# Performance work log

Measured on AMD Instinct MI355X. Metric: run time of the kernel, lower is better.

The kernel has to match this reference:

```python
import jax, jax.numpy as jnp
import numpy as np

SHARED = 128  # matches TabularLoss(shared=128)


def _pairwise_dist(x, y):
    """Batched pairwise L2 distances. x: (B,N,D), y: (B,M,D) -> (B,N,M)."""
    sq = (jnp.sum(x * x, axis=-1)[:, :, None]
          + jnp.sum(y * y, axis=-1)[:, None, :]
          - 2.0 * jnp.einsum('bnd,bmd->bnm', x, y))
    sq = jnp.maximum(sq, 0.0)
    # safe sqrt (exact forward, no NaN grads at 0)
    return jnp.where(sq > 0, jnp.sqrt(jnp.where(sq > 0, sq, 1.0)), 0.0)


def _energy_distance(x, y):
    """geomloss SamplesLoss(loss='energy') with uniform weights.
    L = <a, D_xy b> - 0.5 <a, D_xx a> - 0.5 <b, D_yy b>, a=b=1/N.
    Returns per-batch losses, shape (B,)."""
    dxy = jnp.mean(_pairwise_dist(x, y), axis=(-2, -1))
    dxx = jnp.mean(_pairwise_dist(x, x), axis=(-2, -1))
    dyy = jnp.mean(_pairwise_dist(y, y), axis=(-2, -1))
    return dxy - 0.5 * dxx - 0.5 * dyy


def setup_inputs() -> dict:
    key = jax.random.key(0)
    k1, k2 = jax.random.split(key)
    total, genes = 8192, 5000
    return {
        'input': jax.random.normal(k1, (total, genes), dtype=jnp.float32),
        'target': jax.random.normal(k2, (total, genes), dtype=jnp.float32),
        'downsample': 64,
    }


def reference(input, target, downsample):
    x = input.reshape(-1, downsample, input.shape[-1])   # (B, N, G)
    y = target.reshape(-1, downsample, target.shape[-1])
    # gene-level MMD: each cell group is a point cloud of N cells in G dims
    gene_mmd = jnp.nanmean(_energy_distance(x, y))
    # cell-level MMD: transpose(2,0) -> (S, N, B): per shared gene, N points in B dims
    cx = jnp.transpose(x[:, :, -SHARED:], (2, 1, 0))
    cy = jnp.transpose(y[:, :, -SHARED:], (2, 1, 0))
    cell_mmd = jnp.nanmean(_energy_distance(cx, cy))
    loss = (jnp.where(jnp.isnan(gene_mmd), 0.0, gene_mmd)
            + jnp.where(jnp.isnan(cell_mmd), 0.0, cell_mmd))
    return loss
```

## Files before the change

### kernel.cpp

```cpp
#include <hip/hip_runtime.h>
#include <math.h>

#define TOTAL   8192
#define GENES   5000
#define NDS     64
#define NB      128
#define NSHARED 128
#define KC      64

#define GRAM_OFF 64

typedef __attribute__((ext_vector_type(8)))  short          short8;
typedef __attribute__((ext_vector_type(4)))  unsigned short ushort4v;
typedef __attribute__((ext_vector_type(16))) float          f32x16;

static __device__ inline unsigned short f2bf(float f) {
    unsigned int u = __builtin_bit_cast(unsigned int, f);
    unsigned int r = (u + 0x7fffu + ((u >> 16) & 1u)) >> 16;
    return (unsigned short)r;
}
static __device__ inline float bf2f(unsigned short h) {
    unsigned int u = ((unsigned int)h) << 16;
    return __builtin_bit_cast(float, u);
}

__global__ __launch_bounds__(64) void k_zero(float* ws) {
    ws[threadIdx.x] = 0.0f;
}

__global__ __launch_bounds__(256) void k_gene_gram_mfma(const float* __restrict__ X,
                                                        const float* __restrict__ Y,
                                                        float* __restrict__ grams,
                                                        int splitD, int Dper) {
    const int blk = blockIdx.x;
    const int b = blk / splitD, c = blk % splitD;
    const int d0 = c * Dper;
    const int d1 = min(GENES, d0 + Dper);

    const float* __restrict__ xb = X + (size_t)b * NDS * GENES;
    const float* __restrict__ yb = Y + (size_t)b * NDS * GENES;

    __shared__ __align__(16) unsigned short sXh[NDS * KC], sXl[NDS * KC];
    __shared__ __align__(16) unsigned short sYh[NDS * KC], sYl[NDS * KC];

    const int t    = threadIdx.x;
    const int lane = t & 63;
    const int w    = t >> 6;
    const int qr   = w >> 1, qc = w & 1;
    const int lm   = lane & 31;
    const int kh   = (lane >> 5) << 3;

    const int mr = (qr << 5) + lm;
    const int mc = (qc << 5) + lm;

    f32x16 axy = {0,0,0,0,0,0,0,0,0,0,0,0,0,0,0,0};
    f32x16 axx = {0,0,0,0,0,0,0,0,0,0,0,0,0,0,0,0};
    f32x16 ayy = {0,0,0,0,0,0,0,0,0,0,0,0,0,0,0,0};

    for (int dd0 = d0; dd0 < d1; dd0 += KC) {
        __syncthreads();
#pragma unroll
        for (int it = 0; it < 4; ++it) {
            const int c4 = t & 15;
            const int m  = (t >> 4) + (it << 4);
            const int d  = dd0 + (c4 << 2);
            float vx[4] = {0.f, 0.f, 0.f, 0.f};
            float vy[4] = {0.f, 0.f, 0.f, 0.f};
            if (d + 3 < d1) {
                const float4 fx = *(const float4*)(xb + (size_t)m * GENES + d);
                const float4 fy = *(const float4*)(yb + (size_t)m * GENES + d);
                vx[0]=fx.x; vx[1]=fx.y; vx[2]=fx.z; vx[3]=fx.w;
                vy[0]=fy.x; vy[1]=fy.y; vy[2]=fy.z; vy[3]=fy.w;
            } else if (d < d1) {
                for (int q = 0; q < d1 - d; ++q) {
                    vx[q] = xb[(size_t)m * GENES + d + q];
                    vy[q] = yb[(size_t)m * GENES + d + q];
                }
            }
            ushort4v xh, xl, yh, yl;
#pragma unroll
            for (int q = 0; q < 4; ++q) {
                const unsigned short h = f2bf(vx[q]);
                xh[q] = h; xl[q] = f2bf(vx[q] - bf2f(h));
                const unsigned short g = f2bf(vy[q]);
                yh[q] = g; yl[q] = f2bf(vy[q] - bf2f(g));
            }
            const int e = m * KC + (((c4 << 2)) ^ ((m & 7) << 3));
            *(ushort4v*)&sXh[e] = xh;
            *(ushort4v*)&sXl[e] = xl;
            *(ushort4v*)&sYh[e] = yh;
            *(ushort4v*)&sYl[e] = yl;
        }
        __syncthreads();
#pragma unroll
        for (int ks = 0; ks < 4; ++ks) {
            const int kb = (ks << 4) + kh;
            const int er = mr * KC + (kb ^ ((mr & 7) << 3));
            const int ec = mc * KC + (kb ^ ((mc & 7) << 3));
            const short8 xhr = *(const short8*)&sXh[er];
            const short8 xlr = *(const short8*)&sXl[er];
            const short8 yhr = *(const short8*)&sYh[er];
            const short8 ylr = *(const short8*)&sYl[er];
            const short8 xhc = *(const short8*)&sXh[ec];
            const short8 xlc = *(const short8*)&sXl[ec];
            const short8 yhc = *(const short8*)&sYh[ec];
            const short8 ylc = *(const short8*)&sYl[ec];
            axy = __builtin_amdgcn_mfma_f32_32x32x16_bf16(xhr, yhc, axy, 0, 0, 0);
            axx = __builtin_amdgcn_mfma_f32_32x32x16_bf16(xhr, xhc, axx, 0, 0, 0);
            ayy = __builtin_amdgcn_mfma_f32_32x32x16_bf16(yhr, yhc, ayy, 0, 0, 0);
            axy = __builtin_amdgcn_mfma_f32_32x32x16_bf16(xhr, ylc, axy, 0, 0, 0);
            axx = __builtin_amdgcn_mfma_f32_32x32x16_bf16(xhr, xlc, axx, 0, 0, 0);
            ayy = __builtin_amdgcn_mfma_f32_32x32x16_bf16(yhr, ylc, ayy, 0, 0, 0);
            axy = __builtin_amdgcn_mfma_f32_32x32x16_bf16(xlr, yhc, axy, 0, 0, 0);
            axx = __builtin_amdgcn_mfma_f32_32x32x16_bf16(xlr, xhc, axx, 0, 0, 0);
            ayy = __builtin_amdgcn_mfma_f32_32x32x16_bf16(ylr, yhc, ayy, 0, 0, 0);
        }
    }

    float* g = grams + (size_t)(b * splitD + c) * 3 * 4096;
    const int col = (qc << 5) + lm;
#pragma unroll
    for (int r = 0; r < 16; ++r) {
        const int row = (qr << 5) + (r & 3) + ((r >> 2) << 3) + ((lane >> 5) << 2);
        g[0 * 4096 + row * 64 + col] = axy[r];
        g[1 * 4096 + row * 64 + col] = axx[r];
        g[2 * 4096 + row * 64 + col] = ayy[r];
    }
}

__global__ __launch_bounds__(256) void k_gene_dist(const float* __restrict__ grams,
                                                   float* __restrict__ acc,
                                                   int splitD) {
    const int b = blockIdx.x, t = threadIdx.x;
    __shared__ __align__(16) float G[3 * 4096];
    __shared__ float red[4];

    for (int m = 0; m < 3; ++m) {
#pragma unroll
        for (int k = 0; k < 16; ++k) {
            const int e = t + 256 * k;
            float s = 0.f;
            for (int c = 0; c < splitD; ++c)
                s += grams[((size_t)(b * splitD + c) * 3 + m) * 4096 + e];
            G[m * 4096 + e] = s;
        }
    }
    __syncthreads();

    float local = 0.f;
#pragma unroll
    for (int k = 0; k < 16; ++k) {
        const int e = t + 256 * k;
        const int i = e >> 6, j = e & 63;
        const float gxy = G[e];
        const float gxx = G[4096 + e];
        const float gyy = G[8192 + e];
        const float nxi = G[4096 + i * 65], nxj = G[4096 + j * 65];
        const float nyi = G[8192 + i * 65], nyj = G[8192 + j * 65];
        const float dxy = sqrtf(fmaxf(nxi + nyj - 2.f * gxy, 0.f));
        const float dxx = sqrtf(fmaxf(nxi + nxj - 2.f * gxx, 0.f));
        const float dyy = sqrtf(fmaxf(nyi + nyj - 2.f * gyy, 0.f));
        local += dxy - 0.5f * (dxx + dyy);
    }
#pragma unroll
    for (int off = 32; off; off >>= 1) local += __shfl_down(local, off);
    if ((t & 63) == 0) red[t >> 6] = local;
    __syncthreads();
    if (t == 0) {
        const float bl = red[0] + red[1] + red[2] + red[3];
        atomicAdd(acc, bl * (1.0f / (4096.0f * (float)NB)));
    }
}

__global__ __launch_bounds__(256) void k_cell(const float* __restrict__ X,
                                              const float* __restrict__ Y,
                                              float* __restrict__ acc) {
    const int s   = blockIdx.x;
    const int col = GENES - NSHARED + s;
    const int t   = threadIdx.x;

    __shared__ __align__(16) float lds[16384];

#pragma unroll
    for (int k = 0; k < 32; ++k) {
        const int idx = t + 256 * k;
        lds[idx]        = X[(size_t)idx * GENES + col];
        lds[8192 + idx] = Y[(size_t)idx * GENES + col];
    }
    __syncthreads();

    const int ti = t & 15, tj = t >> 4;
    const int i0 = ti << 2, j0 = tj << 2;
    float axy[4][4] = {{0}}, axx[4][4] = {{0}}, ayy[4][4] = {{0}};

#pragma unroll 4
    for (int bb = 0; bb < NB; ++bb) {
        const float4 xi4 = *(const float4*)(lds + bb * 64 + i0);
        const float4 xj4 = *(const float4*)(lds + bb * 64 + j0);
        const float4 yi4 = *(const float4*)(lds + 8192 + bb * 64 + i0);
        const float4 yj4 = *(const float4*)(lds + 8192 + bb * 64 + j0);
        const float* xi = &xi4.x;
        const float* xj = &xj4.x;
        const float* yi = &yi4.x;
        const float* yj = &yj4.x;
#pragma unroll
        for (int ii = 0; ii < 4; ++ii) {
#pragma unroll
            for (int jj = 0; jj < 4; ++jj) {
                axy[ii][jj] = fmaf(xi[ii], yj[jj], axy[ii][jj]);
                axx[ii][jj] = fmaf(xi[ii], xj[jj], axx[ii][jj]);
                ayy[ii][jj] = fmaf(yi[ii], yj[jj], ayy[ii][jj]);
            }
        }
    }
    __syncthreads();
#pragma unroll
    for (int ii = 0; ii < 4; ++ii) {
        float4 v;
        v.x = axy[ii][0]; v.y = axy[ii][1]; v.z = axy[ii][2]; v.w = axy[ii][3];
        *(float4*)(lds + 0 * 4096 + (i0 + ii) * 64 + j0) = v;
        v.x = axx[ii][0]; v.y = axx[ii][1]; v.z = axx[ii][2]; v.w = axx[ii][3];
        *(float4*)(lds + 1 * 4096 + (i0 + ii) * 64 + j0) = v;
        v.x = ayy[ii][0]; v.y = ayy[ii][1]; v.z = ayy[ii][2]; v.w = ayy[ii][3];
        *(float4*)(lds + 2 * 4096 + (i0 + ii) * 64 + j0) = v;
    }
    __syncthreads();

    float local = 0.f;
#pragma unroll
    for (int k = 0; k < 16; ++k) {
        const int e = t + 256 * k;
        const int i = e >> 6, j = e & 63;
        const float gxy = lds[e];
        const float gxx = lds[4096 + e];
        const float gyy = lds[8192 + e];
        const float nxi = lds[4096 + i * 65], nxj = lds[4096 + j * 65];
        const float nyi = lds[8192 + i * 65], nyj = lds[8192 + j * 65];
        const float dxy = sqrtf(fmaxf(nxi + nyj - 2.f * gxy, 0.f));
        const float dxx = sqrtf(fmaxf(nxi + nxj - 2.f * gxx, 0.f));
        const float dyy = sqrtf(fmaxf(nyi + nyj - 2.f * gyy, 0.f));
        local += dxy - 0.5f * (dxx + dyy);
    }
#pragma unroll
    for (int off = 32; off; off >>= 1) local += __shfl_down(local, off);
    __syncthreads();
    if ((t & 63) == 0) lds[t >> 6] = local;
    __syncthreads();
    if (t == 0) {
        const float bl = lds[0] + lds[1] + lds[2] + lds[3];
        atomicAdd(acc, bl * (1.0f / (4096.0f * (float)NSHARED)));
    }
}

__global__ void k_final(const float* __restrict__ acc, float* __restrict__ out) {
    out[0] = acc[0] + acc[1];
}

extern "C" void kernel_launch(void* const* d_in, const int* in_sizes, int n_in,
                              void* d_out, int out_size, void* d_ws, size_t ws_size,
                              hipStream_t stream) {
    const float* X = (const float*)d_in[0];
    const float* Y = (const float*)d_in[1];
    float* out = (float*)d_out;
    float* ws  = (float*)d_ws;

    int splitD = 4;
    while (splitD > 1 &&
           ((size_t)GRAM_OFF + (size_t)splitD * NB * 3 * 4096) * sizeof(float) > ws_size)
        splitD >>= 1;
    const int chunks = (GENES + KC - 1) / KC;
    const int cper   = (chunks + splitD - 1) / splitD;
    const int Dper   = cper * KC;

    float* acc   = ws;
    float* grams = ws + GRAM_OFF;

    hipLaunchKernelGGL(k_zero,           dim3(1),           dim3(64),  0, stream, acc);
    hipLaunchKernelGGL(k_gene_gram_mfma, dim3(NB * splitD), dim3(256), 0, stream,
                       X, Y, grams, splitD, Dper);
    hipLaunchKernelGGL(k_gene_dist,      dim3(NB),          dim3(256), 0, stream,
                       grams, acc + 0, splitD);
    hipLaunchKernelGGL(k_cell,           dim3(NSHARED),     dim3(256), 0, stream,
                       X, Y, acc + 1);
    hipLaunchKernelGGL(k_final,          dim3(1),           dim3(1),   0, stream, acc, out);
}
```

Before: 192.0 us.

## Prefetch next gene chunk into registers and pre-transpose shared columns for cell kernel

The gene Gram kernel now loads the next KC-wide chunk of X/Y into registers while the current chunk is split into bf16 hi/lo parts and run through the MFMAs, so global load latency overlaps compute. A new transpose kernel copies the last 128 columns of X and Y into a contiguous column-major buffer, reusing the gram workspace, after the gene distance kernel has consumed it. k_cell then does coalesced float4 loads instead of strided per-element column gathers. This adds an extra launch, an extra round trip through global memory, and more register pressure in the Gram kernel.

Result: slower. 235.2 us (+22.5%).

```diff
diff --git a/kernel.cpp b/kernel.cpp
--- a/kernel.cpp
+++ b/kernel.cpp
@@ -53,45 +53,66 @@
     const int mr = (qr << 5) + lm;
     const int mc = (qc << 5) + lm;
 
+    const int c4  = t & 15;
+    const int mrw = t >> 4;
+
     f32x16 axy = {0,0,0,0,0,0,0,0,0,0,0,0,0,0,0,0};
     f32x16 axx = {0,0,0,0,0,0,0,0,0,0,0,0,0,0,0,0};
     f32x16 ayy = {0,0,0,0,0,0,0,0,0,0,0,0,0,0,0,0};
 
-    for (int dd0 = d0; dd0 < d1; dd0 += KC) {
-        __syncthreads();
+    float4 rx[4], ry[4];
+
+    auto load_chunk = [&](int dd0) {
 #pragma unroll
         for (int it = 0; it < 4; ++it) {
-            const int c4 = t & 15;
-            const int m  = (t >> 4) + (it << 4);
-            const int d  = dd0 + (c4 << 2);
-            float vx[4] = {0.f, 0.f, 0.f, 0.f};
-            float vy[4] = {0.f, 0.f, 0.f, 0.f};
+            const int m = mrw + (it << 4);
+            const int d = dd0 + (c4 << 2);
+            float4 vx = {0.f, 0.f, 0.f, 0.f};
+            float4 vy = {0.f, 0.f, 0.f, 0.f};
             if (d + 3 < d1) {
-                const float4 fx = *(const float4*)(xb + (size_t)m * GENES + d);
-                const float4 fy = *(const float4*)(yb + (size_t)m * GENES + d);
-                vx[0]=fx.x; vx[1]=fx.y; vx[2]=fx.z; vx[3]=fx.w;
-                vy[0]=fy.x; vy[1]=fy.y; vy[2]=fy.z; vy[3]=fy.w;
+                vx = *(const float4*)(xb + (size_t)m * GENES + d);
+                vy = *(const float4*)(yb + (size_t)m * GENES + d);
             } else if (d < d1) {
+                float* px = &vx.x; float* py = &vy.x;
                 for (int q = 0; q < d1 - d; ++q) {
-                    vx[q] = xb[(size_t)m * GENES + d + q];
-                    vy[q] = yb[(size_t)m * GENES + d + q];
+                    px[q] = xb[(size_t)m * GENES + d + q];
+                    py[q] = yb[(size_t)m * GENES + d + q];
                 }
             }
-            ushort4v xh, xl, yh, yl;
+            rx[it] = vx; ry[it] = vy;
+        }
+    };
+
+    load_chunk(d0);
+
+    for (int dd0 = d0; dd0 < d1; dd0 += KC) {
+        ushort4v xh[4], xl[4], yh[4], yl[4];
+#pragma unroll
+        for (int it = 0; it < 4; ++it) {
+            const float* px = &rx[it].x;
+            const float* py = &ry[it].x;
 #pragma unroll
             for (int q = 0; q < 4; ++q) {
-                const unsigned short h = f2bf(vx[q]);
-                xh[q] = h; xl[q] = f2bf(vx[q] - bf2f(h));
-                const unsigned short g = f2bf(vy[q]);
-                yh[q] = g; yl[q] = f2bf(vy[q] - bf2f(g));
+                const unsigned short h = f2bf(px[q]);
+                xh[it][q] = h; xl[it][q] = f2bf(px[q] - bf2f(h));
+                const unsigned short g = f2bf(py[q]);
+                yh[it][q] = g; yl[it][q] = f2bf(py[q] - bf2f(g));
             }
-            const int e = m * KC + (((c4 << 2)) ^ ((m & 7) << 3));
-            *(ushort4v*)&sXh[e] = xh;
-            *(ushort4v*)&sXl[e] = xl;
-            *(ushort4v*)&sYh[e] = yh;
-            *(ushort4v*)&sYl[e] = yl;
-        }
+        }
+        if (dd0 + KC < d1) load_chunk(dd0 + KC);
+
         __syncthreads();
+#pragma unroll
+        for (int it = 0; it < 4; ++it) {
+            const int m = mrw + (it << 4);
+            const int e = m * KC + ((c4 << 2) ^ ((m & 7) << 3));
+            *(ushort4v*)&sXh[e] = xh[it];
+            *(ushort4v*)&sXl[e] = xl[it];
+            *(ushort4v*)&sYh[e] = yh[it];
+            *(ushort4v*)&sYl[e] = yl[it];
+        }
+        __syncthreads();
+
 #pragma unroll
         for (int ks = 0; ks < 4; ++ks) {
             const int kb = (ks << 4) + kh;
@@ -172,20 +193,57 @@
     }
 }
 
-__global__ __launch_bounds__(256) void k_cell(const float* __restrict__ X,
-                                              const float* __restrict__ Y,
+__global__ __launch_bounds__(256) void k_transpose(const float* __restrict__ X,
+                                                   const float* __restrict__ Y,
+                                                   float* __restrict__ T) {
+    const int blk = blockIdx.x;
+    const float* __restrict__ src = (blk < NB) ? X : Y;
+    float* __restrict__ dst = T + (size_t)(blk < NB ? 0 : NSHARED * TOTAL);
+    const int rb = (blk & (NB - 1)) * 64;
+    __shared__ float s[NSHARED * 65];
+    const int t = threadIdx.x;
+
+#pragma unroll
+    for (int it = 0; it < 8; ++it) {
+        const int idx = t + 256 * it;
+        const int r = idx >> 5;
+        const int f = idx & 31;
+        const float4 v = *(const float4*)(src + (size_t)(rb + r) * GENES
+                                          + (GENES - NSHARED) + (f << 2));
+        s[((f << 2) + 0) * 65 + r] = v.x;
+        s[((f << 2) + 1) * 65 + r] = v.y;
+        s[((f << 2) + 2) * 65 + r] = v.z;
+        s[((f << 2) + 3) * 65 + r] = v.w;
+    }
+    __syncthreads();
+
+    const int g = t >> 1, h = t & 1;
+#pragma unroll
+    for (int v = 0; v < 8; ++v) {
+        const int r = (h << 5) + (v << 2);
+        float4 o;
+        o.x = s[g * 65 + r + 0];
+        o.y = s[g * 65 + r + 1];
+        o.z = s[g * 65 + r + 2];
+        o.w = s[g * 65 + r + 3];
+        *(float4*)(dst + (size_t)g * TOTAL + rb + r) = o;
+    }
+}
+
+__global__ __launch_bounds__(256) void k_cell(const float* __restrict__ T,
                                               float* __restrict__ acc) {
-    const int s   = blockIdx.x;
-    const int col = GENES - NSHARED + s;
-    const int t   = threadIdx.x;
+    const int s = blockIdx.x;
+    const float* __restrict__ tx = T + (size_t)s * TOTAL;
+    const float* __restrict__ ty = T + (size_t)(NSHARED + s) * TOTAL;
+    const int t = threadIdx.x;
 
     __shared__ __align__(16) float lds[16384];
 
 #pragma unroll
-    for (int k = 0; k < 32; ++k) {
-        const int idx = t + 256 * k;
-        lds[idx]        = X[(size_t)idx * GENES + col];
-        lds[8192 + idx] = Y[(size_t)idx * GENES + col];
+    for (int it = 0; it < 8; ++it) {
+        const int i4 = (t + 256 * it) << 2;
+        *(float4*)&lds[i4]        = *(const float4*)(tx + i4);
+        *(float4*)&lds[8192 + i4] = *(const float4*)(ty + i4);
     }
     __syncthreads();
 
@@ -280,7 +338,9 @@
                        X, Y, grams, splitD, Dper);
     hipLaunchKernelGGL(k_gene_dist,      dim3(NB),          dim3(256), 0, stream,
                        grams, acc + 0, splitD);
+    hipLaunchKernelGGL(k_transpose,      dim3(2 * NB),      dim3(256), 0, stream,
+                       X, Y, grams);
     hipLaunchKernelGGL(k_cell,           dim3(NSHARED),     dim3(256), 0, stream,
-                       X, Y, acc + 1);
+                       grams, acc + 1);
     hipLaunchKernelGGL(k_final,          dim3(1),           dim3(1),   0, stream, acc, out);
 }
```

## Double-buffer LDS tiles and prefetch next chunk into registers during MFMA

Applied to the files above, without the earlier changes.

Adds a second LDS buffer for the bf16 hi/lo split tiles and issues the global loads for the next K-chunk into registers before the current chunk's MFMA work. The loaded data is converted and written to the alternate buffer after the MFMAs, so one barrier per chunk remains instead of two. The aim is to hide global-memory latency behind matrix math. In exchange it doubles LDS usage to 64KB per block and raises register pressure, which may lower occupancy.

New measurement: 225.3 us. +17.3%, slower.

```diff
diff --git a/kernel.cpp b/kernel.cpp
--- a/kernel.cpp
+++ b/kernel.cpp
@@ -40,8 +40,8 @@
     const float* __restrict__ xb = X + (size_t)b * NDS * GENES;
     const float* __restrict__ yb = Y + (size_t)b * NDS * GENES;
 
-    __shared__ __align__(16) unsigned short sXh[NDS * KC], sXl[NDS * KC];
-    __shared__ __align__(16) unsigned short sYh[NDS * KC], sYl[NDS * KC];
+    __shared__ __align__(16) unsigned short sXh[2 * NDS * KC], sXl[2 * NDS * KC];
+    __shared__ __align__(16) unsigned short sYh[2 * NDS * KC], sYl[2 * NDS * KC];
 
     const int t    = threadIdx.x;
     const int lane = t & 63;
@@ -53,50 +53,92 @@
     const int mr = (qr << 5) + lm;
     const int mc = (qc << 5) + lm;
 
+    const int c4  = t & 15;
+    const int mrw = t >> 4;
+    const int dcol = c4 << 2;
+
     f32x16 axy = {0,0,0,0,0,0,0,0,0,0,0,0,0,0,0,0};
     f32x16 axx = {0,0,0,0,0,0,0,0,0,0,0,0,0,0,0,0};
     f32x16 ayy = {0,0,0,0,0,0,0,0,0,0,0,0,0,0,0,0};
 
-    for (int dd0 = d0; dd0 < d1; dd0 += KC) {
-        __syncthreads();
-#pragma unroll
-        for (int it = 0; it < 4; ++it) {
-            const int c4 = t & 15;
-            const int m  = (t >> 4) + (it << 4);
-            const int d  = dd0 + (c4 << 2);
-            float vx[4] = {0.f, 0.f, 0.f, 0.f};
-            float vy[4] = {0.f, 0.f, 0.f, 0.f};
-            if (d + 3 < d1) {
-                const float4 fx = *(const float4*)(xb + (size_t)m * GENES + d);
-                const float4 fy = *(const float4*)(yb + (size_t)m * GENES + d);
-                vx[0]=fx.x; vx[1]=fx.y; vx[2]=fx.z; vx[3]=fx.w;
-                vy[0]=fy.x; vy[1]=fy.y; vy[2]=fy.z; vy[3]=fy.w;
-            } else if (d < d1) {
-                for (int q = 0; q < d1 - d; ++q) {
-                    vx[q] = xb[(size_t)m * GENES + d + q];
-                    vy[q] = yb[(size_t)m * GENES + d + q];
+    float4 rx0, rx1, rx2, rx3, ry0, ry1, ry2, ry3;
+
+    auto issue_loads = [&](int dd0) {
+        const int d = dd0 + dcol;
+        if (d + 3 < d1) {
+            const float* px = xb + (size_t)mrw * GENES + d;
+            const float* py = yb + (size_t)mrw * GENES + d;
+            rx0 = *(const float4*)(px);
+            ry0 = *(const float4*)(py);
+            rx1 = *(const float4*)(px + 16 * GENES);
+            ry1 = *(const float4*)(py + 16 * GENES);
+            rx2 = *(const float4*)(px + 32 * GENES);
+            ry2 = *(const float4*)(py + 32 * GENES);
+            rx3 = *(const float4*)(px + 48 * GENES);
+            ry3 = *(const float4*)(py + 48 * GENES);
+        } else {
+            float4 z = {0.f, 0.f, 0.f, 0.f};
+            rx0 = rx1 = rx2 = rx3 = z;
+            ry0 = ry1 = ry2 = ry3 = z;
+            if (d < d1) {
+                const int nq = d1 - d;
+                float* dstx[4] = {&rx0.x, &rx1.x, &rx2.x, &rx3.x};
+                float* dsty[4] = {&ry0.x, &ry1.x, &ry2.x, &ry3.x};
+#pragma unroll
+                for (int it = 0; it < 4; ++it) {
+                    const size_t base = (size_t)(mrw + (it << 4)) * GENES + d;
+                    for (int q = 0; q < nq; ++q) {
+                        dstx[it][q] = xb[base + q];
+                        dsty[it][q] = yb[base + q];
+                    }
                 }
             }
+        }
+    };
+
+    auto convert_write = [&](int buf) {
+        const int bofs = buf * NDS * KC;
+        const float4 vx[4] = {rx0, rx1, rx2, rx3};
+        const float4 vy[4] = {ry0, ry1, ry2, ry3};
+#pragma unroll
+        for (int it = 0; it < 4; ++it) {
+            const int m = mrw + (it << 4);
+            const float* px = &vx[it].x;
+            const float* py = &vy[it].x;
             ushort4v xh, xl, yh, yl;
 #pragma unroll
             for (int q = 0; q < 4; ++q) {
-                const unsigned short h = f2bf(vx[q]);
-                xh[q] = h; xl[q] = f2bf(vx[q] - bf2f(h));
-                const unsigned short g = f2bf(vy[q]);
-                yh[q] = g; yl[q] = f2bf(vy[q] - bf2f(g));
+                const unsigned short h = f2bf(px[q]);
+                xh[q] = h; xl[q] = f2bf(px[q] - bf2f(h));
+                const unsigned short g = f2bf(py[q]);
+                yh[q] = g; yl[q] = f2bf(py[q] - bf2f(g));
             }
-            const int e = m * KC + (((c4 << 2)) ^ ((m & 7) << 3));
+            const int e = bofs + m * KC + (dcol ^ ((m & 7) << 3));
             *(ushort4v*)&sXh[e] = xh;
             *(ushort4v*)&sXl[e] = xl;
             *(ushort4v*)&sYh[e] = yh;
             *(ushort4v*)&sYl[e] = yl;
         }
+    };
+
+    const int nchunks = (d1 - d0 + KC - 1) / KC;
+
+    issue_loads(d0);
+    convert_write(0);
+
+    for (int ci = 0; ci < nchunks; ++ci) {
+        const int cur = ci & 1;
+        const bool more = (ci + 1 < nchunks);
+        if (more) issue_loads(d0 + (ci + 1) * KC);
+
         __syncthreads();
+
+        const int bofs = cur * NDS * KC;
 #pragma unroll
         for (int ks = 0; ks < 4; ++ks) {
             const int kb = (ks << 4) + kh;
-            const int er = mr * KC + (kb ^ ((mr & 7) << 3));
-            const int ec = mc * KC + (kb ^ ((mc & 7) << 3));
+            const int er = bofs + mr * KC + (kb ^ ((mr & 7) << 3));
+            const int ec = bofs + mc * KC + (kb ^ ((mc & 7) << 3));
             const short8 xhr = *(const short8*)&sXh[er];
             const short8 xlr = *(const short8*)&sXl[er];
             const short8 yhr = *(const short8*)&sYh[er];
@@ -115,6 +157,8 @@
             axx = __builtin_amdgcn_mfma_f32_32x32x16_bf16(xlr, xhc, axx, 0, 0, 0);
             ayy = __builtin_amdgcn_mfma_f32_32x32x16_bf16(ylr, yhc, ayy, 0, 0, 0);
         }
+
+        if (more) convert_write(cur ^ 1);
     }
 
     float* g = grams + (size_t)(b * splitD + c) * 3 * 4096;
```

## Double-buffer gram tiles via direct global-to-LDS loads, split bf16 at fragment load

Applied to the files above, without the earlier changes.

The gram kernel now copies raw fp32 tiles straight from global memory into LDS with global_load_lds and double-buffers them, so the next chunk's load overlaps the current chunk's MFMA work. The hi/lo bf16 split moves from the staging phase to fragment-load time and uses truncation instead of round-to-nearest. Out-of-range lanes read from a zeroed workspace slot instead of taking a scalar tail path. This doubles LDS use, repeats the conversion work per wave, and slightly changes the rounding of the split.

New measurement: 183.6 us. 1.05x faster.

```diff
diff --git a/kernel.cpp b/kernel.cpp
--- a/kernel.cpp
+++ b/kernel.cpp
@@ -10,28 +10,50 @@
 
 #define GRAM_OFF 64
 
-typedef __attribute__((ext_vector_type(8)))  short          short8;
-typedef __attribute__((ext_vector_type(4)))  unsigned short ushort4v;
-typedef __attribute__((ext_vector_type(16))) float          f32x16;
-
-static __device__ inline unsigned short f2bf(float f) {
-    unsigned int u = __builtin_bit_cast(unsigned int, f);
-    unsigned int r = (u + 0x7fffu + ((u >> 16) & 1u)) >> 16;
-    return (unsigned short)r;
-}
-static __device__ inline float bf2f(unsigned short h) {
-    unsigned int u = ((unsigned int)h) << 16;
-    return __builtin_bit_cast(float, u);
-}
+typedef __attribute__((ext_vector_type(8)))  short        short8;
+typedef __attribute__((ext_vector_type(4)))  unsigned int uint4v;
+typedef __attribute__((ext_vector_type(16))) float        f32x16;
+
+typedef const __attribute__((address_space(1))) void* GPTR;
+typedef __attribute__((address_space(3))) void*       LPTR;
+
+#define GLOAD16(gp, lp) \
+    __builtin_amdgcn_global_load_lds((GPTR)(gp), (LPTR)(lp), 16, 0, 0)
 
 __global__ __launch_bounds__(64) void k_zero(float* ws) {
     ws[threadIdx.x] = 0.0f;
 }
 
-__global__ __launch_bounds__(256) void k_gene_gram_mfma(const float* __restrict__ X,
-                                                        const float* __restrict__ Y,
-                                                        float* __restrict__ grams,
-                                                        int splitD, int Dper) {
+static __device__ inline unsigned int hpack(float f0, float f1) {
+    const unsigned int u0 = __builtin_bit_cast(unsigned int, f0);
+    const unsigned int u1 = __builtin_bit_cast(unsigned int, f1);
+    return (u1 & 0xFFFF0000u) | (u0 >> 16);
+}
+static __device__ inline float tbf(float f) {
+    return __builtin_bit_cast(float,
+        __builtin_bit_cast(unsigned int, f) & 0xFFFF0000u);
+}
+struct HL8 { short8 h; short8 l; };
+static __device__ inline HL8 ldcvt(const float* base, int sw, int c0) {
+    const float4 a = *(const float4*)(base + (((c0    ) ^ sw) << 2));
+    const float4 b = *(const float4*)(base + (((c0 + 1) ^ sw) << 2));
+    uint4v hv, lv;
+    hv[0] = hpack(a.x, a.y); hv[1] = hpack(a.z, a.w);
+    hv[2] = hpack(b.x, b.y); hv[3] = hpack(b.z, b.w);
+    lv[0] = hpack(a.x - tbf(a.x), a.y - tbf(a.y));
+    lv[1] = hpack(a.z - tbf(a.z), a.w - tbf(a.w));
+    lv[2] = hpack(b.x - tbf(b.x), b.y - tbf(b.y));
+    lv[3] = hpack(b.z - tbf(b.z), b.w - tbf(b.w));
+    HL8 r;
+    r.h = __builtin_bit_cast(short8, hv);
+    r.l = __builtin_bit_cast(short8, lv);
+    return r;
+}
+
+__global__ __launch_bounds__(256, 2)
+void k_gene_gram_mfma(const float* __restrict__ X, const float* __restrict__ Y,
+                      const float* __restrict__ zsrc,
+                      float* __restrict__ grams, int splitD, int Dper) {
     const int blk = blockIdx.x;
     const int b = blk / splitD, c = blk % splitD;
     const int d0 = c * Dper;
@@ -40,82 +62,96 @@
     const float* __restrict__ xb = X + (size_t)b * NDS * GENES;
     const float* __restrict__ yb = Y + (size_t)b * NDS * GENES;
 
-    __shared__ __align__(16) unsigned short sXh[NDS * KC], sXl[NDS * KC];
-    __shared__ __align__(16) unsigned short sYh[NDS * KC], sYl[NDS * KC];
+    __shared__ __align__(16) float sX[2 * NDS * KC];
+    __shared__ __align__(16) float sY[2 * NDS * KC];
 
     const int t    = threadIdx.x;
     const int lane = t & 63;
     const int w    = t >> 6;
     const int qr   = w >> 1, qc = w & 1;
     const int lm   = lane & 31;
-    const int kh   = (lane >> 5) << 3;
-
-    const int mr = (qr << 5) + lm;
-    const int mc = (qc << 5) + lm;
+    const int kh2  = (lane >> 5) << 1;
+
+    const int mr  = (qr << 5) + lm;
+    const int mc  = (qc << 5) + lm;
+    const int swr = mr & 15, swc = mc & 15;
+
+    const int s16  = lane & 15;
+    const int rsub = lane >> 4;
+    const int rA = (w << 4) + rsub;
+    const int rB = rA + 4, rC = rA + 8, rD = rA + 12;
+    const int cA = (s16 ^ (rA & 15)) << 2;
+    const int cB = (s16 ^ (rB & 15)) << 2;
+    const int cC = (s16 ^ (rC & 15)) << 2;
+    const int cD = (s16 ^ (rD & 15)) << 2;
+    const float* gxA = xb + (size_t)rA * GENES + cA;
+    const float* gxB = xb + (size_t)rB * GENES + cB;
+    const float* gxC = xb + (size_t)rC * GENES + cC;
+    const float* gxD = xb + (size_t)rD * GENES + cD;
+    const float* gyA = yb + (size_t)rA * GENES + cA;
+    const float* gyB = yb + (size_t)rB * GENES + cB;
+    const float* gyC = yb + (size_t)rC * GENES + cC;
+    const float* gyD = yb + (size_t)rD * GENES + cD;
+    const int lA = ((w << 4) + 0) * KC;
+    const int lB = lA + 4 * KC, lC = lA + 8 * KC, lD = lA + 12 * KC;
+
+#define STAGEBUF(bofs, dd) do {                                               \
+    const float* pxA = ((dd) + cA + 4 <= d1) ? gxA + (dd) : zsrc;             \
+    const float* pxB = ((dd) + cB + 4 <= d1) ? gxB + (dd) : zsrc;             \
+    const float* pxC = ((dd) + cC + 4 <= d1) ? gxC + (dd) : zsrc;             \
+    const float* pxD = ((dd) + cD + 4 <= d1) ? gxD + (dd) : zsrc;             \
+    const float* pyA = ((dd) + cA + 4 <= d1) ? gyA + (dd) : zsrc;             \
+    const float* pyB = ((dd) + cB + 4 <= d1) ? gyB + (dd) : zsrc;             \
+    const float* pyC = ((dd) + cC + 4 <= d1) ? gyC + (dd) : zsrc;             \
+    const float* pyD = ((dd) + cD + 4 <= d1) ? gyD + (dd) : zsrc;             \
+    GLOAD16(pxA, sX + (bofs) + lA);                                           \
+    GLOAD16(pxB, sX + (bofs) + lB);                                           \
+    GLOAD16(pxC, sX + (bofs) + lC);                                           \
+    GLOAD16(pxD, sX + (bofs) + lD);                                           \
+    GLOAD16(pyA, sY + (bofs) + lA);                                           \
+    GLOAD16(pyB, sY + (bofs) + lB);                                           \
+    GLOAD16(pyC, sY + (bofs) + lC);                                           \
+    GLOAD16(pyD, sY + (bofs) + lD);                                           \
+} while (0)
 
     f32x16 axy = {0,0,0,0,0,0,0,0,0,0,0,0,0,0,0,0};
     f32x16 axx = {0,0,0,0,0,0,0,0,0,0,0,0,0,0,0,0};
     f32x16 ayy = {0,0,0,0,0,0,0,0,0,0,0,0,0,0,0,0};
 
-    for (int dd0 = d0; dd0 < d1; dd0 += KC) {
-        __syncthreads();
-#pragma unroll
-        for (int it = 0; it < 4; ++it) {
-            const int c4 = t & 15;
-            const int m  = (t >> 4) + (it << 4);
-            const int d  = dd0 + (c4 << 2);
-            float vx[4] = {0.f, 0.f, 0.f, 0.f};
-            float vy[4] = {0.f, 0.f, 0.f, 0.f};
-            if (d + 3 < d1) {
-                const float4 fx = *(const float4*)(xb + (size_t)m * GENES + d);
-                const float4 fy = *(const float4*)(yb + (size_t)m * GENES + d);
-                vx[0]=fx.x; vx[1]=fx.y; vx[2]=fx.z; vx[3]=fx.w;
-                vy[0]=fy.x; vy[1]=fy.y; vy[2]=fy.z; vy[3]=fy.w;
-            } else if (d < d1) {
-                for (int q = 0; q < d1 - d; ++q) {
-                    vx[q] = xb[(size_t)m * GENES + d + q];
-                    vy[q] = yb[(size_t)m * GENES + d + q];
-                }
-            }
-            ushort4v xh, xl, yh, yl;
-#pragma unroll
-            for (int q = 0; q < 4; ++q) {
-                const unsigned short h = f2bf(vx[q]);
-                xh[q] = h; xl[q] = f2bf(vx[q] - bf2f(h));
-                const unsigned short g = f2bf(vy[q]);
-                yh[q] = g; yl[q] = f2bf(vy[q] - bf2f(g));
-            }
-            const int e = m * KC + (((c4 << 2)) ^ ((m & 7) << 3));
-            *(ushort4v*)&sXh[e] = xh;
-            *(ushort4v*)&sXl[e] = xl;
-            *(ushort4v*)&sYh[e] = yh;
-            *(ushort4v*)&sYl[e] = yl;
+    const int nchunks = (d1 - d0 + KC - 1) / KC;
+
+    STAGEBUF(0, d0);
+    __syncthreads();
+
+    for (int ci = 0; ci < nchunks; ++ci) {
+        const int bofs = (ci & 1) * (NDS * KC);
+        if (ci + 1 < nchunks)
+            STAGEBUF(((ci + 1) & 1) * (NDS * KC), d0 + (ci + 1) * KC);
+
+        const float* xrow = sX + bofs + mr * KC;
+        const float* yrow = sY + bofs + mr * KC;
+        const float* xcol = sX + bofs + mc * KC;
+        const float* ycol = sY + bofs + mc * KC;
+#pragma unroll
+        for (int ks = 0; ks < 4; ++ks) {
+            const int c0 = (ks << 2) + kh2;
+            const HL8 xr = ldcvt(xrow, swr, c0);
+            const HL8 yr = ldcvt(yrow, swr, c0);
+            const HL8 xc = ldcvt(xcol, swc, c0);
+            const HL8 yc = ldcvt(ycol, swc, c0);
+            axy = __builtin_amdgcn_mfma_f32_32x32x16_bf16(xr.h, yc.h, axy, 0, 0, 0);
+            axx = __builtin_amdgcn_mfma_f32_32x32x16_bf16(xr.h, xc.h, axx, 0, 0, 0);
+            ayy = __builtin_amdgcn_mfma_f32_32x32x16_bf16(yr.h, yc.h, ayy, 0, 0, 0);
+            axy = __builtin_amdgcn_mfma_f32_32x32x16_bf16(xr.h, yc.l, axy, 0, 0, 0);
+            axx = __builtin_amdgcn_mfma_f32_32x32x16_bf16(xr.h, xc.l, axx, 0, 0, 0);
+            ayy = __builtin_amdgcn_mfma_f32_32x32x16_bf16(yr.h, yc.l, ayy, 0, 0, 0);
+            axy = __builtin_amdgcn_mfma_f32_32x32x16_bf16(xr.l, yc.h, axy, 0, 0, 0);
+            axx = __builtin_amdgcn_mfma_f32_32x32x16_bf16(xr.l, xc.h, axx, 0, 0, 0);
+            ayy = __builtin_amdgcn_mfma_f32_32x32x16_bf16(yr.l, yc.h, ayy, 0, 0, 0);
         }
         __syncthreads();
-#pragma unroll
-        for (int ks = 0; ks < 4; ++ks) {
-            const int kb = (ks << 4) + kh;
-            const int er = mr * KC + (kb ^ ((mr & 7) << 3));
-            const int ec = mc * KC + (kb ^ ((mc & 7) << 3));
-            const short8 xhr = *(const short8*)&sXh[er];
-            const short8 xlr = *(const short8*)&sXl[er];
-            const short8 yhr = *(const short8*)&sYh[er];
-            const short8 ylr = *(const short8*)&sYl[er];
-            const short8 xhc = *(const short8*)&sXh[ec];
-            const short8 xlc = *(const short8*)&sXl[ec];
-            const short8 yhc = *(const short8*)&sYh[ec];
-            const short8 ylc = *(const short8*)&sYl[ec];
-            axy = __builtin_amdgcn_mfma_f32_32x32x16_bf16(xhr, yhc, axy, 0, 0, 0);
-            axx = __builtin_amdgcn_mfma_f32_32x32x16_bf16(xhr, xhc, axx, 0, 0, 0);
-            ayy = __builtin_amdgcn_mfma_f32_32x32x16_bf16(yhr, yhc, ayy, 0, 0, 0);
-            axy = __builtin_amdgcn_mfma_f32_32x32x16_bf16(xhr, ylc, axy, 0, 0, 0);
-            axx = __builtin_amdgcn_mfma_f32_32x32x16_bf16(xhr, xlc, axx, 0, 0, 0);
-            ayy = __builtin_amdgcn_mfma_f32_32x32x16_bf16(yhr, ylc, ayy, 0, 0, 0);
-            axy = __builtin_amdgcn_mfma_f32_32x32x16_bf16(xlr, yhc, axy, 0, 0, 0);
-            axx = __builtin_amdgcn_mfma_f32_32x32x16_bf16(xlr, xhc, axx, 0, 0, 0);
-            ayy = __builtin_amdgcn_mfma_f32_32x32x16_bf16(ylr, yhc, ayy, 0, 0, 0);
-        }
-    }
+    }
+#undef STAGEBUF
 
     float* g = grams + (size_t)(b * splitD + c) * 3 * 4096;
     const int col = (qc << 5) + lm;
@@ -273,11 +309,12 @@
     const int Dper   = cper * KC;
 
     float* acc   = ws;
+    float* zsrc  = ws + 32;
     float* grams = ws + GRAM_OFF;
 
-    hipLaunchKernelGGL(k_zero,           dim3(1),           dim3(64),  0, stream, acc);
+    hipLaunchKernelGGL(k_zero,           dim3(1),           dim3(64),  0, stream, ws);
     hipLaunchKernelGGL(k_gene_gram_mfma, dim3(NB * splitD), dim3(256), 0, stream,
-                       X, Y, grams, splitD, Dper);
+                       X, Y, zsrc, grams, splitD, Dper);
     hipLaunchKernelGGL(k_gene_dist,      dim3(NB),          dim3(256), 0, stream,
                        grams, acc + 0, splitD);
     hipLaunchKernelGGL(k_cell,           dim3(NSHARED),     dim3(256), 0, stream,
```
